# Performance work log

Hardware: AMD Instinct MI355X
Metric: run time of the kernel (lower is better)

The kernel has to match this reference:

```python
import jax, jax.numpy as jnp
import numpy as np

B, C, H, T_IN, T, EPS = 2048, 512, 256, 64, 32, 1e-5


def _interp_linear(x, t_out):
    # torch F.interpolate mode='linear', align_corners=False on [B,C,T]
    t_in = x.shape[-1]
    scale = t_in / t_out
    src = jnp.maximum((jnp.arange(t_out, dtype=jnp.float32) + 0.5) * scale - 0.5, 0.0)
    i0 = jnp.minimum(jnp.floor(src).astype(jnp.int32), t_in - 1)
    i1 = jnp.minimum(i0 + 1, t_in - 1)
    w1 = (src - i0.astype(jnp.float32))
    return x[:, :, i0] * (1.0 - w1) + x[:, :, i1] * w1


def _dwconv(x, w, pad):
    # depthwise conv1d: x [B,C,T], w [C,1,K]
    return jax.lax.conv_general_dilated(
        x, w, window_strides=(1,), padding=[(pad, pad)],
        dimension_numbers=('NCH', 'OIH', 'NCH'), feature_group_count=x.shape[1])


def _bn(x, g, b, m, v):  # eval-mode BatchNorm1d over channel dim of [B,C,T]
    inv = g / jnp.sqrt(v + EPS)
    return (x - m[:, None]) * inv[:, None] + b[:, None]


def _ln(x, g, b):  # LayerNorm over last dim
    mu = x.mean(-1, keepdims=True)
    var = x.var(-1, keepdims=True)
    return (x - mu) / jnp.sqrt(var + EPS) * g + b


def _gelu(x):
    return jax.nn.gelu(x, approximate=False)


def _attn_weights(feats, lg, lb, w1, b1, w2, b2, temp):
    h = _gelu(_ln(feats, lg, lb) @ w1.T + b1)          # [B,T,H]
    s = (h @ w2.T + b2) / jnp.clip(temp, 0.25, 4.0)    # [B,T,1]
    return jax.nn.softmax(s, axis=1)


def setup_inputs() -> dict:
    key = jax.random.key(0)
    ks = jax.random.split(key, 40)
    n = lambda i, shape, s=0.02: jax.random.normal(ks[i], shape, jnp.float32) * s
    u = lambda i, shape: jax.random.uniform(ks[i], shape, jnp.float32, 0.5, 1.5)
    inp = {
        'x': jax.random.normal(ks[0], (B, C, T_IN), jnp.float32),
        'pos_embed': n(1, (1, T, C)),
        'w3': n(2, (C, 1, 3), 0.1),
        'bn3_g': u(3, (C,)), 'bn3_b': n(4, (C,)), 'bn3_m': n(5, (C,)), 'bn3_v': u(6, (C,)),
        'w5': n(7, (C, 1, 5), 0.1),
        'bn5_g': u(8, (C,)), 'bn5_b': n(9, (C,)), 'bn5_m': n(10, (C,)), 'bn5_v': u(11, (C,)),
        'wmix': n(12, (C, 3 * C), 0.02),
        'bnm_g': u(13, (C,)), 'bnm_b': n(14, (C,)), 'bnm_m': n(15, (C,)), 'bnm_v': u(16, (C,)),
        'ln_g': u(17, (C,)), 'ln_b': n(18, (C,)),
        'ed_ln_g': u(19, (C,)), 'ed_ln_b': n(20, (C,)),
        'ed_w1': n(21, (H, C), 0.04), 'ed_b1': n(22, (H,)),
        'ed_w2': n(23, (1, H), 0.06), 'ed_b2': n(24, (1,)),
        'es_ln_g': u(25, (C,)), 'es_ln_b': n(26, (C,)),
        'es_w1': n(27, (H, C), 0.04), 'es_b1': n(28, (H,)),
        'es_w2': n(29, (1, H), 0.06), 'es_b2': n(30, (1,)),
        'temp_ed': jnp.float32(1.0), 'temp_es': jnp.float32(1.0),
    }
    return inp


def reference(x, pos_embed, w3, bn3_g, bn3_b, bn3_m, bn3_v, w5, bn5_g, bn5_b, bn5_m, bn5_v,
              wmix, bnm_g, bnm_b, bnm_m, bnm_v, ln_g, ln_b,
              ed_ln_g, ed_ln_b, ed_w1, ed_b1, ed_w2, ed_b2,
              es_ln_g, es_ln_b, es_w1, es_b1, es_w2, es_b2, temp_ed, temp_es):
    tf = _interp_linear(x, T)                                 # [B,C,T]
    c3 = _gelu(_bn(_dwconv(tf, w3, 1), bn3_g, bn3_b, bn3_m, bn3_v))
    c5 = _gelu(_bn(_dwconv(tf, w5, 2), bn5_g, bn5_b, bn5_m, bn5_v))
    cat = jnp.concatenate([tf, c3, c5], axis=1)               # [B,3C,T]
    ctx = _gelu(_bn(jnp.einsum('bct,oc->bot', cat, wmix), bnm_g, bnm_b, bnm_m, bnm_v))
    feats = _ln(tf.transpose(0, 2, 1) + ctx.transpose(0, 2, 1) + pos_embed, ln_g, ln_b)  # [B,T,C]
    aw_ed = _attn_weights(feats, ed_ln_g, ed_ln_b, ed_w1, ed_b1, ed_w2, ed_b2, temp_ed)
    aw_es = _attn_weights(feats, es_ln_g, es_ln_b, es_w1, es_b1, es_w2, es_b2, temp_es)
    pair = jnp.concatenate([aw_ed, aw_es], axis=-1)           # [B,T,2]
    w_mean = pair.mean(axis=-1, keepdims=True)                # [B,T,1]
    pooled = (feats * w_mean).sum(axis=1)                     # [B,C]
    return feats, pooled, pair
```

## Files before the change

### kernel.cpp

```cpp
#include <hip/hip_runtime.h>
#include <cstdint>

typedef __bf16 bf16;
typedef __attribute__((ext_vector_type(8))) __bf16 bf16x8;
typedef __attribute__((ext_vector_type(4))) float f32x4;

#define CEPS 1e-5f
#define MROWS 65536
#define NB 2048
#define CDIM 512
#define K3C 1536
#define MKT 24

__device__ __forceinline__ float gelu_f(float x) {
  float x2 = x * x;
  float u = x * (0.7978845608f + 0.0356774081f * x2);
  float e = __expf(2.0f * u);
  float th = 1.0f - __fdividef(2.0f, e + 1.0f);
  return 0.5f * x * (1.0f + th);
}

__device__ __forceinline__ void gload_lds16(const void* g, void* l) {
  using GP = const __attribute__((address_space(1))) void*;
  using LP = __attribute__((address_space(3))) void*;
  __builtin_amdgcn_global_load_lds(reinterpret_cast<GP>(reinterpret_cast<uintptr_t>(g)),
                                   reinterpret_cast<LP>(reinterpret_cast<uintptr_t>(l)),
                                   16, 0, 0);
}

__device__ __forceinline__ int xcd_swz(int bid, int nwg) {
  int q = nwg >> 3, r = nwg & 7;
  int xcd = bid & 7, i = bid >> 3;
  return (xcd < r ? xcd * (q + 1) : r * (q + 1) + (xcd - r) * q) + i;
}

__global__ __launch_bounds__(256) void fold_kernel(
    const float* __restrict__ wmix, const float* __restrict__ bnm_g, const float* __restrict__ bnm_v,
    const float* __restrict__ edg, const float* __restrict__ edb,
    const float* __restrict__ esg, const float* __restrict__ esb,
    const float* __restrict__ w1a, const float* __restrict__ w1b,
    const float* __restrict__ b1a, const float* __restrict__ b1b,
    bf16* __restrict__ wmixf, bf16* __restrict__ w1f, float* __restrict__ b1f) {
  __shared__ float red[4];
  int bid = blockIdx.x, tid = threadIdx.x;
  if (bid < 512) {
    int o = bid;
    float s = bnm_g[o] * rsqrtf(bnm_v[o] + CEPS);
    for (int c = tid; c < K3C; c += 256)
      wmixf[(size_t)o * K3C + c] = (bf16)(wmix[(size_t)o * K3C + c] * s);
  } else {
    int n = bid - 512;
    int half = (n < 256) ? 0 : 1;
    const float* g  = half ? esg : edg;
    const float* lb = half ? esb : edb;
    const float* w1 = half ? w1b : w1a;
    const float* b1 = half ? b1b : b1a;
    int nn = n & 255;
    float dot = 0.f;
    for (int c = tid; c < 512; c += 256) {
      float w = w1[(size_t)nn * 512 + c];
      w1f[(size_t)n * 512 + c] = (bf16)(w * g[c]);
      dot += w * lb[c];
    }
    #pragma unroll
    for (int off = 1; off < 64; off <<= 1) dot += __shfl_xor(dot, off, 64);
    if ((tid & 63) == 0) red[tid >> 6] = dot;
    __syncthreads();
    if (tid == 0) b1f[n] = b1[nn] + red[0] + red[1] + red[2] + red[3];
  }
}

__global__ __launch_bounds__(512) void prep_kernel(
    const float* __restrict__ x,
    const float* __restrict__ w3, const float* __restrict__ bn3g, const float* __restrict__ bn3b,
    const float* __restrict__ bn3m, const float* __restrict__ bn3v,
    const float* __restrict__ w5, const float* __restrict__ bn5g, const float* __restrict__ bn5b,
    const float* __restrict__ bn5m, const float* __restrict__ bn5v,
    bf16* __restrict__ Acat) {
  int b = blockIdx.x, c = threadIdx.x;
  const float4* xp = (const float4*)(x + ((size_t)b * 512 + c) * 64);
  float tf[32];
  #pragma unroll
  for (int i = 0; i < 16; i++) {
    float4 v = xp[i];
    tf[2 * i]     = 0.5f * (v.x + v.y);
    tf[2 * i + 1] = 0.5f * (v.z + v.w);
  }
  float s3 = bn3g[c] * rsqrtf(bn3v[c] + CEPS), t3 = bn3b[c] - bn3m[c] * s3;
  float s5 = bn5g[c] * rsqrtf(bn5v[c] + CEPS), t5 = bn5b[c] - bn5m[c] * s5;
  float w30 = w3[c * 3], w31 = w3[c * 3 + 1], w32 = w3[c * 3 + 2];
  float w50 = w5[c * 5], w51 = w5[c * 5 + 1], w52 = w5[c * 5 + 2], w53 = w5[c * 5 + 3], w54 = w5[c * 5 + 4];
  bf16* Ab = Acat + (size_t)b * 32 * K3C + c;
  #pragma unroll
  for (int t = 0; t < 32; t++) {
    float tm2 = (t >= 2) ? tf[t - 2] : 0.f;
    float tm1 = (t >= 1) ? tf[t - 1] : 0.f;
    float tp1 = (t < 31) ? tf[t + 1] : 0.f;
    float tp2 = (t < 30) ? tf[t + 2] : 0.f;
    float c3 = gelu_f((w30 * tm1 + w31 * tf[t] + w32 * tp1) * s3 + t3);
    float c5 = gelu_f((w50 * tm2 + w51 * tm1 + w52 * tf[t] + w53 * tp1 + w54 * tp2) * s5 + t5);
    Ab[t * K3C]        = (bf16)tf[t];
    Ab[t * K3C + 512]  = (bf16)c3;
    Ab[t * K3C + 1024] = (bf16)c5;
  }
}

#define MFMA1 __builtin_amdgcn_mfma_f32_16x16x32_bf16

#define PHASE(q)                                                              \
  {                                                                           \
    bf16x8 Bf[2][2];                                                          \
    _Pragma("unroll")                                                         \
    for (int i = 0; i < 2; i++) {                                             \
      Bf[i][0] = *(const bf16x8*)(lds + sl + bOff0 + (q) * 16384 + i * 2048); \
      Bf[i][1] = *(const bf16x8*)(lds + sl + bOff1 + (q) * 16384 + i * 2048); \
    }                                                                         \
    __builtin_amdgcn_s_barrier();                                             \
    __builtin_amdgcn_s_setprio(1);                                            \
    _Pragma("unroll")                                                         \
    for (int k2 = 0; k2 < 2; k2++)                                            \
      _Pragma("unroll")                                                       \
      for (int i = 0; i < 2; i++)                                             \
        _Pragma("unroll")                                                     \
        for (int mr = 0; mr < 4; mr++)                                        \
          acc[mr][2 * (q) + i] = MFMA1(Af[mr][k2], Bf[i][k2], acc[mr][2 * (q) + i], 0, 0, 0); \
    __builtin_amdgcn_s_setprio(0);                                            \
    if (stB) stageBq(sl, (q), t + 2);                                         \
  }

__global__ __launch_bounds__(512, 1) void mega_kernel(
    const bf16* __restrict__ Acat, const bf16* __restrict__ Bw, const bf16* __restrict__ w1f,
    const float* __restrict__ bn_g, const float* __restrict__ bn_b,
    const float* __restrict__ bn_m, const float* __restrict__ bn_v,
    const float* __restrict__ pos, const float* __restrict__ lng, const float* __restrict__ lnb,
    const float* __restrict__ b1f, const float* __restrict__ w2a, const float* __restrict__ w2b,
    const float* __restrict__ ta, const float* __restrict__ tb,
    float* __restrict__ feats, float* __restrict__ pair, float* __restrict__ pooled) {
  __shared__ char lds[163840];
  int tid = threadIdx.x;
  int wv = tid >> 6, lane = tid & 63;
  int wm = wv >> 2, wn = wv & 3;
  int fr = lane & 15, kq = lane >> 4;
  int mb = xcd_swz(blockIdx.x, gridDim.x);

  const size_t AKB = 3072;
  const char* Ablk = (const char*)Acat + (size_t)mb * 128 * AKB;

  int r8 = tid >> 3;
  int colx = ((tid & 7) << 4) ^ ((r8 & 7) << 4);
  const char* pA = Ablk + (size_t)r8 * AKB + colx;
  int r32 = r8 & 31, st0 = r8 >> 5;
  const char* pB = (const char*)Bw + (size_t)(st0 * 128 + r32) * AKB
                 + (((tid & 7) << 4) ^ ((r32 & 7) << 4));
  const int dstIdx = tid * 16;

  int e0 = (kq << 4) ^ ((fr & 7) << 4);
  int e1 = (64 | (kq << 4)) ^ ((fr & 7) << 4);
  int aB_ = (wm * 64 + fr) * 128;
  int bB_ = 16384 + (wn * 32 + fr) * 128;
  const int aOff0 = aB_ + e0, aOff1 = aB_ + e1;
  const int bOff0 = bB_ + e0, bOff1 = bB_ + e1;

  auto stageA = [&](int slot, int t) {
    char* d = lds + slot + dstIdx;
    const char* s = pA + (size_t)t * 128;
    gload_lds16(s, d);
    gload_lds16(s + 64 * AKB, d + 8192);
  };
  auto stageBq = [&](int slot, int q, int t) {
    char* d = lds + slot + 16384 + q * 16384 + dstIdx;
    const char* s = pB + (size_t)q * 32 * AKB + (size_t)t * 128;
    gload_lds16(s, d);
    gload_lds16(s + 256 * AKB, d + 8192);
  };

  const f32x4 fz = {0.f, 0.f, 0.f, 0.f};
  f32x4 acc[4][8];
  #pragma unroll
  for (int i = 0; i < 4; i++)
    #pragma unroll
    for (int j = 0; j < 8; j++) acc[i][j] = fz;

  stageA(0, 0);
  #pragma unroll
  for (int q = 0; q < 4; q++) stageBq(0, q, 0);
  #pragma unroll
  for (int q = 0; q < 4; q++) stageBq(81920, q, 1);
  asm volatile("s_waitcnt vmcnt(8)" ::: "memory");
  __builtin_amdgcn_s_barrier();

  for (int t = 0; t < MKT; t++) {
    const int sl = (t & 1) * 81920;
    const bool stA = (t + 1 < MKT), stB = (t + 2 < MKT);
    if (stA) stageA(sl ^ 81920, t + 1);
    bf16x8 Af[4][2];
    #pragma unroll
    for (int mr = 0; mr < 4; mr++) {
      Af[mr][0] = *(const bf16x8*)(lds + sl + aOff0 + mr * 2048);
      Af[mr][1] = *(const bf16x8*)(lds + sl + aOff1 + mr * 2048);
    }
    PHASE(0);
    __builtin_amdgcn_s_barrier();
    PHASE(1);
    __builtin_amdgcn_s_barrier();
    PHASE(2);
    __builtin_amdgcn_s_barrier();
    PHASE(3);
    if (t < MKT - 2) {
      asm volatile("s_waitcnt vmcnt(8)" ::: "memory");
    } else if (t == MKT - 2) {
      asm volatile("s_waitcnt vmcnt(0)" ::: "memory");
    }
    __builtin_amdgcn_s_barrier();
  }

  {
    float biasm[8];
    #pragma unroll
    for (int nr = 0; nr < 8; nr++) {
      int n = wn * 128 + nr * 16 + fr;
      float s = bn_g[n] * rsqrtf(bn_v[n] + CEPS);
      biasm[nr] = bn_b[n] - bn_m[n] * s;
    }
    #pragma unroll
    for (int mr = 0; mr < 4; mr++)
      #pragma unroll
      for (int nr = 0; nr < 8; nr++)
        #pragma unroll
        for (int j = 0; j < 4; j++)
          acc[mr][nr][j] = gelu_f(acc[mr][nr][j] + biasm[nr]);
  }
  __syncthreads();
  {
    const char* ptf = Ablk + (size_t)wv * AKB + ((lane * 16) ^ (wv << 4));
    char* d = lds + wv * 1024 + lane * 16;
    #pragma unroll
    for (int l = 0; l < 16; l++) gload_lds16(ptf + (size_t)l * 8 * AKB, d + l * 8192);
  }
  __syncthreads();
  float* sst  = (float*)(lds + 131072);
  float* minv = (float*)(lds + 135168);
  {
    float s1[4][4], s2[4][4];
    #pragma unroll
    for (int mr = 0; mr < 4; mr++)
      #pragma unroll
      for (int j = 0; j < 4; j++) { s1[mr][j] = 0.f; s2[mr][j] = 0.f; }
    #pragma unroll
    for (int mr = 0; mr < 4; mr++)
      #pragma unroll
      for (int j = 0; j < 4; j++) {
        int r = wm * 64 + mr * 16 + kq * 4 + j;
        int swz = (r & 7) << 4;
        #pragma unroll
        for (int nr = 0; nr < 8; nr++) {
          int c = wn * 128 + nr * 16 + fr;
          float tfv = (float)*(const bf16*)(lds + r * 1024 + ((c * 2) ^ swz));
          float z = acc[mr][nr][j] + tfv + pos[(r & 31) * 512 + c];
          acc[mr][nr][j] = z;
          s1[mr][j] += z; s2[mr][j] += z * z;
        }
      }
    #pragma unroll
    for (int mr = 0; mr < 4; mr++)
      #pragma unroll
      for (int j = 0; j < 4; j++)
        #pragma unroll
        for (int off = 1; off < 16; off <<= 1) {
          s1[mr][j] += __shfl_xor(s1[mr][j], off, 64);
          s2[mr][j] += __shfl_xor(s2[mr][j], off, 64);
        }
    if (fr == 0) {
      #pragma unroll
      for (int mr = 0; mr < 4; mr++)
        #pragma unroll
        for (int j = 0; j < 4; j++) {
          int r = wm * 64 + mr * 16 + kq * 4 + j;
          ((float2*)sst)[r * 4 + wn] = make_float2(s1[mr][j], s2[mr][j]);
        }
    }
  }
  __syncthreads();
  if (tid < 128) {
    float a = 0.f, b = 0.f;
    #pragma unroll
    for (int w = 0; w < 4; w++) { float2 v = ((float2*)sst)[tid * 4 + w]; a += v.x; b += v.y; }
    float mu = a * (1.f / 512.f);
    float var = b * (1.f / 512.f) - mu * mu;
    ((float2*)minv)[tid] = make_float2(mu, rsqrtf(var + CEPS));
  }
  __syncthreads();
  {
    float g_[8], b_[8];
    #pragma unroll
    for (int nr = 0; nr < 8; nr++) {
      int c = wn * 128 + nr * 16 + fr;
      g_[nr] = lng[c]; b_[nr] = lnb[c];
    }
    float t1[4][4], t2[4][4];
    #pragma unroll
    for (int mr = 0; mr < 4; mr++)
      #pragma unroll
      for (int j = 0; j < 4; j++) { t1[mr][j] = 0.f; t2[mr][j] = 0.f; }
    #pragma unroll
    for (int mr = 0; mr < 4; mr++)
      #pragma unroll
      for (int j = 0; j < 4; j++) {
        int r = wm * 64 + mr * 16 + kq * 4 + j;
        float2 mi = ((float2*)minv)[r];
        #pragma unroll
        for (int nr = 0; nr < 8; nr++) {
          int c = wn * 128 + nr * 16 + fr;
          float f = (acc[mr][nr][j] - mi.x) * mi.y * g_[nr] + b_[nr];
          acc[mr][nr][j] = f;
          feats[((size_t)mb * 128 + r) * 512 + c] = f;
          t1[mr][j] += f; t2[mr][j] += f * f;
        }
      }
    #pragma unroll
    for (int mr = 0; mr < 4; mr++)
      #pragma unroll
      for (int j = 0; j < 4; j++)
        #pragma unroll
        for (int off = 1; off < 16; off <<= 1) {
          t1[mr][j] += __shfl_xor(t1[mr][j], off, 64);
          t2[mr][j] += __shfl_xor(t2[mr][j], off, 64);
        }
    if (fr == 0) {
      #pragma unroll
      for (int mr = 0; mr < 4; mr++)
        #pragma unroll
        for (int j = 0; j < 4; j++) {
          int r = wm * 64 + mr * 16 + kq * 4 + j;
          ((float2*)sst)[r * 4 + wn] = make_float2(t1[mr][j], t2[mr][j]);
        }
    }
  }
  __syncthreads();
  if (tid < 128) {
    float a = 0.f, b = 0.f;
    #pragma unroll
    for (int w = 0; w < 4; w++) { float2 v = ((float2*)sst)[tid * 4 + w]; a += v.x; b += v.y; }
    float mu = a * (1.f / 512.f);
    float var = b * (1.f / 512.f) - mu * mu;
    ((float2*)minv)[tid] = make_float2(mu, rsqrtf(var + CEPS));
  }
  __syncthreads();
  #pragma unroll
  for (int mr = 0; mr < 4; mr++)
    #pragma unroll
    for (int j = 0; j < 4; j++) {
      int r = wm * 64 + mr * 16 + kq * 4 + j;
      int swz = (r & 7) << 4;
      float2 mi = ((float2*)minv)[r];
      #pragma unroll
      for (int nr = 0; nr < 8; nr++) {
        int c = wn * 128 + nr * 16 + fr;
        *(bf16*)(lds + r * 1024 + ((c * 2) ^ swz)) = (bf16)((acc[mr][nr][j] - mi.x) * mi.y);
      }
    }
  __syncthreads();
  float2 miKeep = make_float2(0.f, 1.f);
  if (tid < 128) miKeep = ((float2*)minv)[tid];
  __syncthreads();
  #pragma unroll
  for (int i = 0; i < 4; i++)
    #pragma unroll
    for (int j = 0; j < 8; j++) acc[i][j] = fz;
  float b1l[8], w2l[8];
  #pragma unroll
  for (int h = 0; h < 2; h++) {
    float tv = fminf(fmaxf(h ? tb[0] : ta[0], 0.25f), 4.0f);
    #pragma unroll
    for (int nr = 0; nr < 4; nr++) {
      int np = wn * 64 + nr * 16 + fr;
      b1l[h * 4 + nr] = b1f[h * 256 + np];
      w2l[h * 4 + nr] = (h ? w2b[np] : w2a[np]) / tv;
    }
  }
  {
    const char* pW = (const char*)w1f + (size_t)r8 * 1024 + colx;
    int azB = (wm * 64 + fr) * 1024;
    int abB = 131072 + (wn * 64 + fr) * 128;
    const int azOff0 = azB + e0, azOff1 = azB + e1;
    const int abOff0 = abB + e0, abOff1 = abB + e1;
    #pragma unroll
    for (int h = 0; h < 2; h++) {
      {
        char* d = lds + 131072 + dstIdx;
        #pragma unroll
        for (int l = 0; l < 4; l++)
          gload_lds16(pW + h * 262144 + l * 65536, d + l * 8192);
      }
      __syncthreads();
      for (int kk = 0; kk < 8; kk++) {
        bf16x8 pf[4];
        if (kk < 7) {
          #pragma unroll
          for (int l = 0; l < 4; l++)
            pf[l] = *(const bf16x8*)(pW + h * 262144 + l * 65536 + (kk + 1) * 128);
        }
        bf16x8 Az[4][2], Bz[4][2];
        #pragma unroll
        for (int mr = 0; mr < 4; mr++) {
          Az[mr][0] = *(const bf16x8*)(lds + azOff0 + mr * 16384 + kk * 128);
          Az[mr][1] = *(const bf16x8*)(lds + azOff1 + mr * 16384 + kk * 128);
        }
        #pragma unroll
        for (int nr = 0; nr < 4; nr++) {
          Bz[nr][0] = *(const bf16x8*)(lds + abOff0 + nr * 2048);
          Bz[nr][1] = *(const bf16x8*)(lds + abOff1 + nr * 2048);
        }
        __builtin_amdgcn_s_setprio(1);
        #pragma unroll
        for (int k2 = 0; k2 < 2; k2++)
          #pragma unroll
          for (int mr = 0; mr < 4; mr++)
            #pragma unroll
            for (int nr = 0; nr < 4; nr++)
              acc[mr][h * 4 + nr] = MFMA1(Az[mr][k2], Bz[nr][k2], acc[mr][h * 4 + nr], 0, 0, 0);
        __builtin_amdgcn_s_setprio(0);
        if (kk < 7) {
          __syncthreads();
          char* d = lds + 131072 + dstIdx;
          #pragma unroll
          for (int l = 0; l < 4; l++) *(bf16x8*)(d + l * 8192) = pf[l];
          __syncthreads();
        }
      }
      __syncthreads();
    }
  }
  float* sstE = (float*)(lds + 131072);
  float* sstS = (float*)(lds + 133120);
  {
    float pE[4][4], pS[4][4];
    #pragma unroll
    for (int mr = 0; mr < 4; mr++)
      #pragma unroll
      for (int j = 0; j < 4; j++) { pE[mr][j] = 0.f; pS[mr][j] = 0.f; }
    #pragma unroll
    for (int mr = 0; mr < 4; mr++)
      #pragma unroll
      for (int j = 0; j < 4; j++)
        #pragma unroll
        for (int q8 = 0; q8 < 8; q8++) {
          float hh = gelu_f(acc[mr][q8][j] + b1l[q8]) * w2l[q8];
          if (q8 < 4) pE[mr][j] += hh; else pS[mr][j] += hh;
        }
    #pragma unroll
    for (int mr = 0; mr < 4; mr++)
      #pragma unroll
      for (int j = 0; j < 4; j++)
        #pragma unroll
        for (int off = 1; off < 16; off <<= 1) {
          pE[mr][j] += __shfl_xor(pE[mr][j], off, 64);
          pS[mr][j] += __shfl_xor(pS[mr][j], off, 64);
        }
    if (fr == 0) {
      #pragma unroll
      for (int mr = 0; mr < 4; mr++)
        #pragma unroll
        for (int j = 0; j < 4; j++) {
          int r = wm * 64 + mr * 16 + kq * 4 + j;
          sstE[r * 4 + wn] = pE[mr][j];
          sstS[r * 4 + wn] = pS[mr][j];
        }
    }
  }
  __syncthreads();
  float* wmu = (float*)(lds + 136192);
  float* mvv = (float*)(lds + 136704);
  float* vb  = (float*)(lds + 137216);
  if (tid < 128) {
    float vE = sstE[tid * 4] + sstE[tid * 4 + 1] + sstE[tid * 4 + 2] + sstE[tid * 4 + 3];
    float vS = sstS[tid * 4] + sstS[tid * 4 + 1] + sstS[tid * 4 + 2] + sstS[tid * 4 + 3];
    float mE = vE, mS = vS;
    #pragma unroll
    for (int off = 1; off < 32; off <<= 1) {
      mE = fmaxf(mE, __shfl_xor(mE, off, 32));
      mS = fmaxf(mS, __shfl_xor(mS, off, 32));
    }
    float eE = __expf(vE - mE), eS = __expf(vS - mS);
    float sumE = eE, sumS = eS;
    #pragma unroll
    for (int off = 1; off < 32; off <<= 1) {
      sumE += __shfl_xor(sumE, off, 32);
      sumS += __shfl_xor(sumS, off, 32);
    }
    float awE = eE / sumE, awS = eS / sumS;
    size_t pidx = ((size_t)mb * 128 + tid) * 2;
    pair[pidx] = awE;
    pair[pidx + 1] = awS;
    float w = 0.5f * (awE + awS);
    wmu[tid] = __fdividef(w, miKeep.y);
    mvv[tid] = w * miKeep.x;
  }
  __syncthreads();
  if (tid < 4) {
    float s = 0.f;
    #pragma unroll
    for (int i = 0; i < 32; i++) s += mvv[tid * 32 + i];
    vb[tid] = s;
  }
  __syncthreads();
  {
    int c = tid;
    float ps[4] = {0.f, 0.f, 0.f, 0.f};
    #pragma unroll 8
    for (int r = 0; r < 128; r++) {
      float zv = (float)*(const bf16*)(lds + r * 1024 + ((c * 2) ^ ((r & 7) << 4)));
      ps[r >> 5] += zv * wmu[r];
    }
    #pragma unroll
    for (int b = 0; b < 4; b++)
      pooled[(size_t)(mb * 4 + b) * 512 + c] = ps[b] + vb[b];
  }
}

extern "C" void kernel_launch(void* const* d_in, const int* in_sizes, int n_in,
                              void* d_out, int out_size, void* d_ws, size_t ws_size,
                              hipStream_t stream) {
  const float* x     = (const float*)d_in[0];
  const float* pos   = (const float*)d_in[1];
  const float* w3    = (const float*)d_in[2];
  const float* bn3g  = (const float*)d_in[3];
  const float* bn3b  = (const float*)d_in[4];
  const float* bn3m  = (const float*)d_in[5];
  const float* bn3v  = (const float*)d_in[6];
  const float* w5    = (const float*)d_in[7];
  const float* bn5g  = (const float*)d_in[8];
  const float* bn5b  = (const float*)d_in[9];
  const float* bn5m  = (const float*)d_in[10];
  const float* bn5v  = (const float*)d_in[11];
  const float* wmix  = (const float*)d_in[12];
  const float* bnmg  = (const float*)d_in[13];
  const float* bnmb  = (const float*)d_in[14];
  const float* bnmm  = (const float*)d_in[15];
  const float* bnmv  = (const float*)d_in[16];
  const float* lng   = (const float*)d_in[17];
  const float* lnb   = (const float*)d_in[18];
  const float* edlng = (const float*)d_in[19];
  const float* edlnb = (const float*)d_in[20];
  const float* edw1  = (const float*)d_in[21];
  const float* edb1  = (const float*)d_in[22];
  const float* edw2  = (const float*)d_in[23];
  const float* eslng = (const float*)d_in[25];
  const float* eslnb = (const float*)d_in[26];
  const float* esw1  = (const float*)d_in[27];
  const float* esb1  = (const float*)d_in[28];
  const float* esw2  = (const float*)d_in[29];
  const float* ted   = (const float*)d_in[31];
  const float* tes   = (const float*)d_in[32];

  char* ws = (char*)d_ws;
  bf16* Acat  = (bf16*)ws;
  bf16* wmixf = (bf16*)(ws + 201326592);
  bf16* w1f   = (bf16*)(ws + 202899456);
  float* b1f  = (float*)(ws + 203423744);

  float* feats  = (float*)d_out;
  float* pooled = feats + 33554432;
  float* pair   = pooled + 1048576;

  fold_kernel<<<1024, 256, 0, stream>>>(wmix, bnmg, bnmv, edlng, edlnb, eslng, eslnb,
                                        edw1, esw1, edb1, esb1, wmixf, w1f, b1f);
  prep_kernel<<<NB, 512, 0, stream>>>(x, w3, bn3g, bn3b, bn3m, bn3v,
                                      w5, bn5g, bn5b, bn5m, bn5v, Acat);
  mega_kernel<<<MROWS / 128, 512, 0, stream>>>(
      Acat, wmixf, w1f, bnmg, bnmb, bnmm, bnmv, pos, lng, lnb,
      b1f, edw2, esw2, ted, tes, feats, pair, pooled);
}
```

Baseline: 371.5 us.

## Read tf and W1 directly from global, drop LDS staging and barriers

Fuses the BN+GELU epilogue into the residual/LN-stat loop and reads the tf residual directly from global memory rather than first copying the A block into LDS. The attention-MLP GEMM now loads W1 fragments straight from global into registers each k-step, removing the LDS double-staging and its per-iteration barriers. The intent is to cut synchronisation and LDS traffic. The cost is uncoalesced scalar bf16 global reads for tf and more global/L2 load latency exposed inside the MFMA loop. Extra barriers are added before the stats writes to protect the reused LDS region, and minv is kept live rather than copied to a register early.

```diff
diff --git a/kernel.cpp b/kernel.cpp
--- a/kernel.cpp
+++ b/kernel.cpp
@@ -214,6 +214,8 @@
     __builtin_amdgcn_s_barrier();
   }
 
+  float* sst  = (float*)(lds + 131072);
+  float* minv = (float*)(lds + 135168);
   {
     float biasm[8];
     #pragma unroll
@@ -222,25 +224,7 @@
       float s = bn_g[n] * rsqrtf(bn_v[n] + CEPS);
       biasm[nr] = bn_b[n] - bn_m[n] * s;
     }
-    #pragma unroll
-    for (int mr = 0; mr < 4; mr++)
-      #pragma unroll
-      for (int nr = 0; nr < 8; nr++)
-        #pragma unroll
-        for (int j = 0; j < 4; j++)
-          acc[mr][nr][j] = gelu_f(acc[mr][nr][j] + biasm[nr]);
-  }
-  __syncthreads();
-  {
-    const char* ptf = Ablk + (size_t)wv * AKB + ((lane * 16) ^ (wv << 4));
-    char* d = lds + wv * 1024 + lane * 16;
-    #pragma unroll
-    for (int l = 0; l < 16; l++) gload_lds16(ptf + (size_t)l * 8 * AKB, d + l * 8192);
-  }
-  __syncthreads();
-  float* sst  = (float*)(lds + 131072);
-  float* minv = (float*)(lds + 135168);
-  {
+    const bf16* AblkT = (const bf16*)Ablk;
     float s1[4][4], s2[4][4];
     #pragma unroll
     for (int mr = 0; mr < 4; mr++)
@@ -251,12 +235,12 @@
       #pragma unroll
       for (int j = 0; j < 4; j++) {
         int r = wm * 64 + mr * 16 + kq * 4 + j;
-        int swz = (r & 7) << 4;
+        const bf16* tfrow = AblkT + (size_t)r * K3C;
+        const float* posrow = pos + (r & 31) * 512;
         #pragma unroll
         for (int nr = 0; nr < 8; nr++) {
           int c = wn * 128 + nr * 16 + fr;
-          float tfv = (float)*(const bf16*)(lds + r * 1024 + ((c * 2) ^ swz));
-          float z = acc[mr][nr][j] + tfv + pos[(r & 31) * 512 + c];
+          float z = gelu_f(acc[mr][nr][j] + biasm[nr]) + (float)tfrow[c] + posrow[c];
           acc[mr][nr][j] = z;
           s1[mr][j] += z; s2[mr][j] += z * z;
         }
@@ -270,6 +254,7 @@
           s1[mr][j] += __shfl_xor(s1[mr][j], off, 64);
           s2[mr][j] += __shfl_xor(s2[mr][j], off, 64);
         }
+    __syncthreads();
     if (fr == 0) {
       #pragma unroll
       for (int mr = 0; mr < 4; mr++)
@@ -326,6 +311,7 @@
           t1[mr][j] += __shfl_xor(t1[mr][j], off, 64);
           t2[mr][j] += __shfl_xor(t2[mr][j], off, 64);
         }
+    __syncthreads();
     if (fr == 0) {
       #pragma unroll
       for (int mr = 0; mr < 4; mr++)
@@ -360,9 +346,6 @@
       }
     }
   __syncthreads();
-  float2 miKeep = make_float2(0.f, 1.f);
-  if (tid < 128) miKeep = ((float2*)minv)[tid];
-  __syncthreads();
   #pragma unroll
   for (int i = 0; i < 4; i++)
     #pragma unroll
@@ -379,37 +362,24 @@
     }
   }
   {
-    const char* pW = (const char*)w1f + (size_t)r8 * 1024 + colx;
+    const char* pWb = (const char*)w1f + (size_t)(wn * 64 + fr) * 1024 + (kq << 4);
     int azB = (wm * 64 + fr) * 1024;
-    int abB = 131072 + (wn * 64 + fr) * 128;
     const int azOff0 = azB + e0, azOff1 = azB + e1;
-    const int abOff0 = abB + e0, abOff1 = abB + e1;
     #pragma unroll
     for (int h = 0; h < 2; h++) {
-      {
-        char* d = lds + 131072 + dstIdx;
-        #pragma unroll
-        for (int l = 0; l < 4; l++)
-          gload_lds16(pW + h * 262144 + l * 65536, d + l * 8192);
-      }
-      __syncthreads();
+      #pragma unroll 2
       for (int kk = 0; kk < 8; kk++) {
-        bf16x8 pf[4];
-        if (kk < 7) {
-          #pragma unroll
-          for (int l = 0; l < 4; l++)
-            pf[l] = *(const bf16x8*)(pW + h * 262144 + l * 65536 + (kk + 1) * 128);
-        }
         bf16x8 Az[4][2], Bz[4][2];
+        #pragma unroll
+        for (int nr = 0; nr < 4; nr++) {
+          const char* p = pWb + h * 262144 + nr * 16384 + kk * 128;
+          Bz[nr][0] = *(const bf16x8*)p;
+          Bz[nr][1] = *(const bf16x8*)(p + 64);
+        }
         #pragma unroll
         for (int mr = 0; mr < 4; mr++) {
           Az[mr][0] = *(const bf16x8*)(lds + azOff0 + mr * 16384 + kk * 128);
           Az[mr][1] = *(const bf16x8*)(lds + azOff1 + mr * 16384 + kk * 128);
-        }
-        #pragma unroll
-        for (int nr = 0; nr < 4; nr++) {
-          Bz[nr][0] = *(const bf16x8*)(lds + abOff0 + nr * 2048);
-          Bz[nr][1] = *(const bf16x8*)(lds + abOff1 + nr * 2048);
         }
         __builtin_amdgcn_s_setprio(1);
         #pragma unroll
@@ -420,15 +390,7 @@
             for (int nr = 0; nr < 4; nr++)
               acc[mr][h * 4 + nr] = MFMA1(Az[mr][k2], Bz[nr][k2], acc[mr][h * 4 + nr], 0, 0, 0);
         __builtin_amdgcn_s_setprio(0);
-        if (kk < 7) {
-          __syncthreads();
-          char* d = lds + 131072 + dstIdx;
-          #pragma unroll
-          for (int l = 0; l < 4; l++) *(bf16x8*)(d + l * 8192) = pf[l];
-          __syncthreads();
-        }
       }
-      __syncthreads();
     }
   }
   float* sstE = (float*)(lds + 131072);
@@ -493,8 +455,9 @@
     pair[pidx] = awE;
     pair[pidx + 1] = awS;
     float w = 0.5f * (awE + awS);
-    wmu[tid] = __fdividef(w, miKeep.y);
-    mvv[tid] = w * miKeep.x;
+    float2 mi = ((float2*)minv)[tid];
+    wmu[tid] = __fdividef(w, mi.y);
+    mvv[tid] = w * mi.x;
   }
   __syncthreads();
   if (tid < 4) {
```

New measurement: 382.7 us. 3.0% more time.

## Load W1 B-fragments directly from global into registers, drop LDS staging

Applied to the files above, without the earlier changes.

The attention-MLP GEMM no longer stages W1 tiles through LDS with per-k-step barriers. Each wave now loads its B fragments straight from global memory (L2-resident weights) into registers, double-buffered one k-step ahead, and the mean/invstd values are re-read from LDS later rather than kept live across the GEMM. This removes LDS writes and several __syncthreads per k-step, at the cost of redundant global loads across waves and more register pressure. An extra barrier is added before the stats write, apparently to avoid an LDS reuse hazard.

```diff
diff --git a/kernel.cpp b/kernel.cpp
--- a/kernel.cpp
+++ b/kernel.cpp
@@ -326,6 +326,7 @@
           t1[mr][j] += __shfl_xor(t1[mr][j], off, 64);
           t2[mr][j] += __shfl_xor(t2[mr][j], off, 64);
         }
+    __syncthreads();
     if (fr == 0) {
       #pragma unroll
       for (int mr = 0; mr < 4; mr++)
@@ -360,9 +361,6 @@
       }
     }
   __syncthreads();
-  float2 miKeep = make_float2(0.f, 1.f);
-  if (tid < 128) miKeep = ((float2*)minv)[tid];
-  __syncthreads();
   #pragma unroll
   for (int i = 0; i < 4; i++)
     #pragma unroll
@@ -379,37 +377,32 @@
     }
   }
   {
-    const char* pW = (const char*)w1f + (size_t)r8 * 1024 + colx;
+    const char* pWb = (const char*)w1f + (size_t)(wn * 64 + fr) * 1024 + (kq << 4);
     int azB = (wm * 64 + fr) * 1024;
-    int abB = 131072 + (wn * 64 + fr) * 128;
     const int azOff0 = azB + e0, azOff1 = azB + e1;
-    const int abOff0 = abB + e0, abOff1 = abB + e1;
     #pragma unroll
     for (int h = 0; h < 2; h++) {
-      {
-        char* d = lds + 131072 + dstIdx;
-        #pragma unroll
-        for (int l = 0; l < 4; l++)
-          gload_lds16(pW + h * 262144 + l * 65536, d + l * 8192);
+      const char* pH = pWb + h * 262144;
+      bf16x8 Bc[4][2], Bn[4][2];
+      #pragma unroll
+      for (int nr = 0; nr < 4; nr++) {
+        Bc[nr][0] = *(const bf16x8*)(pH + nr * 16384);
+        Bc[nr][1] = *(const bf16x8*)(pH + nr * 16384 + 64);
       }
-      __syncthreads();
+      #pragma unroll
       for (int kk = 0; kk < 8; kk++) {
-        bf16x8 pf[4];
         if (kk < 7) {
           #pragma unroll
-          for (int l = 0; l < 4; l++)
-            pf[l] = *(const bf16x8*)(pW + h * 262144 + l * 65536 + (kk + 1) * 128);
-        }
-        bf16x8 Az[4][2], Bz[4][2];
+          for (int nr = 0; nr < 4; nr++) {
+            Bn[nr][0] = *(const bf16x8*)(pH + nr * 16384 + (kk + 1) * 128);
+            Bn[nr][1] = *(const bf16x8*)(pH + nr * 16384 + (kk + 1) * 128 + 64);
+          }
+        }
+        bf16x8 Az[4][2];
         #pragma unroll
         for (int mr = 0; mr < 4; mr++) {
           Az[mr][0] = *(const bf16x8*)(lds + azOff0 + mr * 16384 + kk * 128);
           Az[mr][1] = *(const bf16x8*)(lds + azOff1 + mr * 16384 + kk * 128);
-        }
-        #pragma unroll
-        for (int nr = 0; nr < 4; nr++) {
-          Bz[nr][0] = *(const bf16x8*)(lds + abOff0 + nr * 2048);
-          Bz[nr][1] = *(const bf16x8*)(lds + abOff1 + nr * 2048);
         }
         __builtin_amdgcn_s_setprio(1);
         #pragma unroll
@@ -418,17 +411,11 @@
           for (int mr = 0; mr < 4; mr++)
             #pragma unroll
             for (int nr = 0; nr < 4; nr++)
-              acc[mr][h * 4 + nr] = MFMA1(Az[mr][k2], Bz[nr][k2], acc[mr][h * 4 + nr], 0, 0, 0);
+              acc[mr][h * 4 + nr] = MFMA1(Az[mr][k2], Bc[nr][k2], acc[mr][h * 4 + nr], 0, 0, 0);
         __builtin_amdgcn_s_setprio(0);
-        if (kk < 7) {
-          __syncthreads();
-          char* d = lds + 131072 + dstIdx;
-          #pragma unroll
-          for (int l = 0; l < 4; l++) *(bf16x8*)(d + l * 8192) = pf[l];
-          __syncthreads();
-        }
+        #pragma unroll
+        for (int nr = 0; nr < 4; nr++) { Bc[nr][0] = Bn[nr][0]; Bc[nr][1] = Bn[nr][1]; }
       }
-      __syncthreads();
     }
   }
   float* sstE = (float*)(lds + 131072);
@@ -493,8 +480,9 @@
     pair[pidx] = awE;
     pair[pidx + 1] = awS;
     float w = 0.5f * (awE + awS);
-    wmu[tid] = __fdividef(w, miKeep.y);
-    mvv[tid] = w * miKeep.x;
+    float2 mi = ((float2*)minv)[tid];
+    wmu[tid] = __fdividef(w, mi.y);
+    mvv[tid] = w * mi.x;
   }
   __syncthreads();
   if (tid < 4) {
```

After: 389.7 us. 1.05x slower.
